# Performance work log

Hardware: AMD Instinct MI355X
Metric: run time of the kernel (lower is better)

Reference implementation:

```python
import jax, jax.numpy as jnp
import numpy as np

N_OBJS = 100          # max detections / scatter buffer size
TOP_K = 100           # top_k_n peaks per channel
KP_THRES = 0.3        # score threshold before NMS
NMS_IOU = 0.5
RESIZE_H, RESIZE_W = 1536.0, 1536.0   # resize_shape (== heatmap HxW here)
H, W = 1536, 1536


def _peak_hms(hms):
    # 3x3 stride-1 SAME max pool; keep only local maxima (Base.apply_max_pool)
    hmax = jax.lax.reduce_window(hms, -jnp.inf, jax.lax.max, (1, 3, 3, 1), (1, 1, 1, 1), 'SAME')
    return jnp.where(hms == hmax, hms, 0.0)


def _top_k_loc(hms, k):
    # per-channel top-k peak coordinates -> [b, c, k, 2] (y, x) int32
    b, h, w, c = hms.shape
    flat = jnp.transpose(hms, (0, 3, 1, 2)).reshape(b, c, h * w)
    _, idx = jax.lax.top_k(flat, k)
    return jnp.stack([idx // w, idx % w], axis=-1).astype(jnp.int32)


def _iou_matrix(boxes):
    # boxes [N,4] = (y1,x1,y2,x2)
    y1, x1, y2, x2 = boxes[:, 0], boxes[:, 1], boxes[:, 2], boxes[:, 3]
    area = jnp.maximum(y2 - y1, 0.0) * jnp.maximum(x2 - x1, 0.0)
    iy1 = jnp.maximum(y1[:, None], y1[None, :]); ix1 = jnp.maximum(x1[:, None], x1[None, :])
    iy2 = jnp.minimum(y2[:, None], y2[None, :]); ix2 = jnp.minimum(x2[:, None], x2[None, :])
    inter = jnp.maximum(iy2 - iy1, 0.0) * jnp.maximum(ix2 - ix1, 0.0)
    union = area[:, None] + area[None, :] - inter
    return inter / jnp.maximum(union, 1e-8)


def _nms_single(boxes, scores):
    # greedy single-class NMS, fixed-size (combined_non_max_suppression equivalent,
    # clip_boxes=False, score_threshold=-inf); padded slots are zeros like TF.
    order = jnp.argsort(-scores)
    boxes, scores = boxes[order], scores[order]
    n = boxes.shape[0]
    iou = _iou_matrix(boxes)
    idxs = jnp.arange(n)

    def step(suppressed, inp):
        i, iou_row = inp
        keep_i = ~suppressed[i]
        return suppressed | (keep_i & (iou_row > NMS_IOU) & (idxs > i)), keep_i

    _, keep = jax.lax.scan(step, jnp.zeros(n, bool), (idxs, iou))
    perm = jnp.argsort(jnp.where(keep, 0, 1))  # stable: compact kept to front, score order preserved
    keep_s = keep[perm]
    out_boxes = jnp.where(keep_s[:, None], boxes[perm], 0.0)
    out_scores = jnp.where(keep_s, scores[perm], 0.0)
    return out_boxes, out_scores, jnp.zeros(n, jnp.float32)


def _forward(obj_heat_map, offset_map, size_maps, origin_shapes):
    resize_shape = jnp.array([RESIZE_H, RESIZE_W], jnp.float32)
    ratio = origin_shapes / resize_shape                      # [b,2]
    hms = _peak_hms(obj_heat_map)                             # [b,H,W,2]
    b = hms.shape[0]
    coors = _top_k_loc(hms, TOP_K)                            # [b,2,K,2]
    b_coors, b_lnmks = coors[:, :1], coors[:, 1:]             # obj / nose coords
    bidx = jnp.arange(b)[:, None, None]

    # nose landmark: scores at nose-channel peaks, masked mean of coords (int mean like TF)
    nose_scores = hms[bidx, b_lnmks[..., 0], b_lnmks[..., 1], 1]     # [b,1,K]
    nose_mask = nose_scores > 0.5
    cnt = jnp.maximum(jnp.sum(nose_mask), 1)
    lnmk_mean = jnp.sum(jnp.where(nose_mask[..., None], b_lnmks, 0), axis=(0, 1, 2)) // cnt
    b_lnmks_m = lnmk_mean.reshape(b, 1, 2)                    # requires b == 1 (as in original)
    b_nose_scores = jnp.where(nose_mask, nose_scores, -1.0).reshape(b, -1)

    # boxes from sizes at object peaks
    size_vals = size_maps[bidx, b_coors[..., 0], b_coors[..., 1]]    # [b,1,K,2]
    obj_scores = hms[bidx, b_coors[..., 0], b_coors[..., 1], 0]      # [b,1,K]
    centers = b_coors.astype(jnp.float32)
    tls = jnp.maximum(centers - size_vals / 2.0, 0.0)
    brs = jnp.minimum(centers + size_vals / 2.0, resize_shape - 1.0)
    bboxes = jnp.concatenate([tls, brs], axis=-1) * jnp.tile(ratio, (1, 2))[:, None, None, :]
    bboxes, scores = bboxes[:, 0], obj_scores[:, 0]           # [b,K,4], [b,K]

    # scatter masked candidates into -1-initialized buffer (tensor_scatter_nd_update equivalent)
    mask = scores > KP_THRES
    cand = jnp.where(mask[..., None], jnp.concatenate([bboxes, scores[..., None]], -1), -1.0)
    cand = jnp.pad(cand, ((0, 0), (0, N_OBJS - TOP_K), (0, 0)), constant_values=-1.0)  # [b,N_OBJS,5]

    nb, ns, nc = jax.vmap(_nms_single)(cand[..., :4], cand[..., 4])
    box_results = jnp.where(nb == -1.0, jnp.inf, nb)
    box_results = jnp.where(box_results == 0.0, jnp.inf, box_results)  # (x - 1 == -1)
    b_bboxes = jnp.concatenate([box_results, ns[..., None], nc[..., None]], axis=-1)  # [b,N_OBJS,6]

    # offset vectors at the mean nose landmark (gather 8ch -> [b,n,4,2])
    bidx2 = jnp.arange(b)[:, None]
    off = offset_map[bidx2, b_lnmks_m[..., 0], b_lnmks_m[..., 1]].reshape(b, 1, 4, 2)
    lf = b_lnmks_m.astype(jnp.float32)
    b_ENM = (lf[:, :, None, :] - off) * ratio[:, None, None, :]
    b_lnmks_out = lf * ratio[:, None, :]
    return b_bboxes, b_lnmks_out, b_ENM, b_nose_scores


def setup_inputs() -> dict:
    key = jax.random.key(0)
    k1, k2, k3 = jax.random.split(key, 3)
    obj_heat_map = jax.random.uniform(k1, (1, H, W, 2), jnp.float32)
    offset_map = jax.random.normal(k2, (1, H, W, 8), jnp.float32) * 8.0
    size_maps = jax.random.uniform(k3, (1, H, W, 2), jnp.float32) * 128.0
    origin_shapes = jnp.array([[1080.0, 1920.0]], jnp.float32)
    return {"obj_heat_map": obj_heat_map, "offset_map": offset_map,
            "size_maps": size_maps, "origin_shapes": origin_shapes}


def reference(obj_heat_map, offset_map, size_maps, origin_shapes):
    return _forward(obj_heat_map, offset_map, size_maps, origin_shapes)
```

## Files before the change

kernel.cpp:

```cpp
#include <hip/hip_runtime.h>
#include <cstdint>

#define IW 1536
#define IH 1536
#define TOPK 100
#define CAPP 327680
#define CAPB 128
#define CAPT 8192
#define BF_INF16 0x7F7Fu

typedef unsigned u32; typedef unsigned long long u64; typedef unsigned short u16;

#define OH1   0
#define OH2   512
#define OSEL  1024
#define OCNT  1032
#define OLB   1040
#define OLT   1552
#define OPK   17936

__device__ __forceinline__ u32 enc16(u32 b){ b &= 0xFFFFu; return (b & 0x8000u) ? ((~b)&0xFFFFu) : (b|0x8000u); }
__device__ __forceinline__ u32 dec16(u32 e){ return (e & 0x8000u) ? (e^0x8000u) : ((~e)&0xFFFFu); }
__device__ __forceinline__ float up16(u32 b){ return __uint_as_float((b&0xFFFFu)<<16); }
__device__ __forceinline__ u16 f2bf(float f){ u32 u=__float_as_uint(f); return (u16)((u + 0x7FFFu + ((u>>16)&1u))>>16); }

__global__ __launch_bounds__(1024) void scan_kernel(const u32* __restrict__ hm, u32* __restrict__ ws){
  __shared__ u32 lh[512];
  __shared__ u32 lbuf[2][1600];
  __shared__ u32 lcnt[2], lbase[2];
  int tid = threadIdx.x, lane = tid & 63;
  for(int i=tid;i<512;i+=1024) lh[i]=0u;
  if(tid<2) lcnt[tid]=0u;
  __syncthreads();

  int p = (blockIdx.x*1024 + tid)*4;
  int y = p / IW, x = p - y*IW;
  const u32* R1 = hm + y*IW;
  const u32* R0 = y ? R1 - IW : R1;
  const u32* R2 = (y < IH-1) ? R1 + IW : R1;
  uint4 c0 = *(const uint4*)(R0+x), c1 = *(const uint4*)(R1+x), c2 = *(const uint4*)(R2+x);
  int xl = x ? x-1 : 0, xr = (x+4 < IW) ? x+4 : IW-1;
  u32 a0[6] = {R0[xl], c0.x, c0.y, c0.z, c0.w, R0[xr]};
  u32 a1[6] = {R1[xl], c1.x, c1.y, c1.z, c1.w, R1[xr]};
  u32 a2[6] = {R2[xl], c2.x, c2.y, c2.z, c2.w, R2[xr]};

  #pragma unroll
  for(int j=0;j<4;++j){
    u32 c = a1[j+1];
    u32 cl = c & 0xFFFFu, chv = c >> 16;
    u32 m0=0u, m1=0u;
    #pragma unroll
    for(int d=0;d<3;++d){
      u32 n0=a0[j+d], n2=a2[j+d];
      u32 t;
      t=n0&0xFFFFu; m0=t>m0?t:m0;  t=n0>>16; m1=t>m1?t:m1;
      t=n2&0xFFFFu; m0=t>m0?t:m0;  t=n2>>16; m1=t>m1?t:m1;
    }
    { u32 n=a1[j]; u32 t=n&0xFFFFu; m0=t>m0?t:m0; t=n>>16; m1=t>m1?t:m1; }
    { u32 n=a1[j+2]; u32 t=n&0xFFFFu; m0=t>m0?t:m0; t=n>>16; m1=t>m1?t:m1; }
    bool p0 = (cl >= m0), p1 = (chv >= m1);

    u64 mk0 = __ballot(p0);
    if(mk0){
      u32 cntw = __popcll(mk0), b;
      if(lane==0) b = atomicAdd(&lcnt[0], cntw);
      b = __shfl(b, 0);
      if(p0){
        u32 pos = b + __popcll(mk0 & ((1ull<<lane)-1ull));
        if(pos < 1600) lbuf[0][pos] = (u32)(p+j);
      }
    }
    u64 mk1 = __ballot(p1);
    if(mk1){
      u32 cntw = __popcll(mk1), b;
      if(lane==0) b = atomicAdd(&lcnt[1], cntw);
      b = __shfl(b, 0);
      if(p1){
        u32 pos = b + __popcll(mk1 & ((1ull<<lane)-1ull));
        if(pos < 1600) lbuf[1][pos] = (u32)(p+j);
      }
    }
    if(p0) atomicAdd(&lh[enc16(cl)>>8], 1u);
    if(p1) atomicAdd(&lh[256 + (enc16(chv)>>8)], 1u);
  }
  __syncthreads();
  if(tid < 2){
    u32 n = lcnt[tid]; if(n > 1600) n = 1600;
    lcnt[tid] = n;
    lbase[tid] = atomicAdd(&ws[OCNT+tid], n);
  }
  __syncthreads();
  for(int ch=0;ch<2;++ch){
    u32 n = lcnt[ch], base = lbase[ch];
    for(u32 i=tid;i<n;i+=1024){
      u32 g = base + i;
      if(g < CAPP) ws[OPK + ch*CAPP + g] = lbuf[ch][i];
    }
  }
  for(int i=tid;i<512;i+=1024) if(lh[i]) atomicAdd(&ws[OH1+i], lh[i]);
}

__global__ void sel_msd_kernel(u32* __restrict__ ws){
  __shared__ u32 h[512];
  int t = threadIdx.x;
  h[t] = ws[OH1+t];
  __syncthreads();
  if(t < 2){
    const u32* hh = h + t*256;
    u32 above = 0; int D = 0;
    for(int b=255;b>=1;--b){
      if(above + hh[b] >= (u32)TOPK){ D = b; break; }
      above += hh[b];
    }
    ws[OSEL+t] = (u32)D;
    ws[OSEL+2+t] = above;
  }
}

__global__ __launch_bounds__(1024) void lsd_kernel(const u32* __restrict__ hm, u32* __restrict__ ws){
  __shared__ u32 lh[512];
  int tid = threadIdx.x;
  for(int i=tid;i<512;i+=1024) lh[i]=0u;
  __syncthreads();
  int D0 = (int)ws[OSEL], D1 = (int)ws[OSEL+1];
  for(int ch=0;ch<2;++ch){
    u32 n = ws[OCNT+ch]; if(n > CAPP) n = CAPP;
    int D = ch ? D1 : D0;
    for(u32 i = blockIdx.x*1024 + tid; i < n; i += gridDim.x*1024){
      u32 idx = ws[OPK + ch*CAPP + i];
      u32 e = enc16(hm[idx] >> (16*ch));
      if((int)(e>>8) == D) atomicAdd(&lh[ch*256 + (e&255)], 1u);
    }
  }
  __syncthreads();
  for(int i=tid;i<512;i+=1024) if(lh[i]) atomicAdd(&ws[OH2+i], lh[i]);
}

__global__ void sel_lsd_kernel(u32* __restrict__ ws){
  __shared__ u32 h[512];
  int t = threadIdx.x;
  h[t] = ws[OH2+t];
  __syncthreads();
  if(t < 2){
    int D = (int)ws[OSEL+t];
    int need2 = TOPK - (int)ws[OSEL+2+t];
    const u32* hh = h + t*256;
    u32 above = 0; int L = 0;
    for(int b=255;b>=1;--b){
      if((int)(above + hh[b]) >= need2){ L = b; break; }
      above += hh[b];
    }
    ws[OSEL+4+t] = (u32)((D<<8) | L);
  }
}

__global__ __launch_bounds__(1024) void collect_kernel(const u32* __restrict__ hm, u32* __restrict__ ws){
  __shared__ u32 tbuf[2][2048];
  __shared__ u32 tcnt[2], tbase[2];
  int tid = threadIdx.x, lane = tid & 63;
  if(tid<2) tcnt[tid]=0u;
  __syncthreads();
  u32 thr0 = ws[OSEL+4], thr1 = ws[OSEL+5];
  u64* listB = (u64*)(ws + OLB);
  u32 total = gridDim.x*1024;
  for(int ch=0;ch<2;++ch){
    u32 n = ws[OCNT+ch]; if(n > CAPP) n = CAPP;
    u32 thr = ch ? thr1 : thr0;
    for(u32 base = blockIdx.x*1024; base < n; base += total){
      u32 i = base + tid;
      bool act = (i < n);
      u32 idx = 0, e = 0;
      if(act){ idx = ws[OPK + ch*CAPP + i]; e = enc16(hm[idx] >> (16*ch)); }
      if(act && e > thr){
        u32 pos = atomicAdd(&ws[OCNT+2+ch], 1u);
        if(pos < CAPB) listB[ch*CAPB + pos] = ((u64)e<<32) | (u32)(~idx);
      }
      bool isT = act && (e == thr);
      u64 mk = __ballot(isT);
      if(mk){
        u32 cntw = __popcll(mk), b;
        if(lane==0) b = atomicAdd(&tcnt[ch], cntw);
        b = __shfl(b, 0);
        if(isT){
          u32 pos = b + __popcll(mk & ((1ull<<lane)-1ull));
          if(pos < 2048) tbuf[ch][pos] = idx;
        }
      }
    }
  }
  __syncthreads();
  if(tid < 2){
    u32 c = tcnt[tid]; if(c > 2048) c = 2048;
    tcnt[tid] = c;
    tbase[tid] = atomicAdd(&ws[OCNT+4+tid], c);
  }
  __syncthreads();
  for(int ch=0;ch<2;++ch)
    for(u32 i=tid;i<tcnt[ch];i+=1024){
      u32 g = tbase[ch] + i;
      if(g < CAPT) ws[OLT + ch*CAPT + g] = tbuf[ch][i];
    }
}

__global__ __launch_bounds__(1024) void finalize_kernel(
    u32* __restrict__ ws, const u32* __restrict__ szm, const u16* __restrict__ offm,
    const u16* __restrict__ orig, u16* __restrict__ out){
  __shared__ u32 cnts[8];
  __shared__ u64 keysL[CAPB];
  __shared__ u32 h2[2048];
  __shared__ u32 wbits[64];
  __shared__ u32 sel[CAPB];
  __shared__ int Bv, cntBelowS, selc;
  __shared__ float oval[TOPK]; __shared__ int oidx[TOPK];
  __shared__ float nval[TOPK]; __shared__ int nidx[TOPK];
  __shared__ float cbox[TOPK][4]; __shared__ float cscore[TOPK]; __shared__ float area[TOPK];
  __shared__ int sup[TOPK]; __shared__ int slotv[TOPK];
  __shared__ u64 nbits[2*TOPK];
  __shared__ u64 suppS[2];
  __shared__ int cS, srS, scS, meanr, meanc;
  int tid = threadIdx.x, lane = tid & 63;
  const u64* listB = (const u64*)(ws + OLB);

  if(tid < 6) cnts[tid] = ws[OCNT+tid];
  if(tid < 2) cnts[6+tid] = ws[OSEL+4+tid];
  if(tid < TOPK){ oval[tid]=0.0f; oidx[tid]=0; nval[tid]=0.0f; nidx[tid]=0; }
  __syncthreads();

  for(int ch=0; ch<2; ++ch){
    int nB = (int)cnts[2+ch]; if(nB > CAPB) nB = CAPB; if(nB > TOPK) nB = TOPK;
    u32 thr = cnts[6+ch];
    float tval = up16(dec16(thr));
    float* dval = ch ? nval : oval;
    int*   didx = ch ? nidx : oidx;

    u64 kreg = 0;
    if(tid < nB){ kreg = listB[ch*CAPB + tid]; keysL[tid] = kreg; }
    for(int i=tid;i<2048;i+=1024) h2[i]=0u;
    if(tid < 64) wbits[tid]=0u;
    if(tid == 0){ selc = 0; Bv = 0; cntBelowS = 0; }
    __syncthreads();
    if(tid < nB){
      int r = 0;
      for(int j=0;j<nB;++j) r += (keysL[j] > kreg);
      dval[r] = up16(dec16((u32)(kreg>>32)));
      didx[r] = (int)(~(u32)(kreg & 0xFFFFFFFFu));
    }
    int need = TOPK - nB;

    if(need > 0){
      int nT = (int)cnts[4+ch]; if(nT > CAPT) nT = CAPT;
      const u32* seg = ws + OLT + ch*CAPT;
      for(int i=tid;i<nT;i+=1024) atomicAdd(&h2[seg[i]>>11], 1u);
      __syncthreads();
      if(tid < 64){
        int base = tid*32;
        u32 s = 0;
        #pragma unroll
        for(int k2=0;k2<32;++k2) s += h2[base+k2];
        u32 c = s;
        #pragma unroll
        for(int off=1;off<64;off<<=1){
          u32 v = __shfl_up(c, off, 64);
          if(lane >= off) c += v;
        }
        u64 m = __ballot(c >= (u32)need);
        int L = (int)(__ffsll((unsigned long long)m) - 1);
        if(tid == L){
          u32 cum2 = c - s;
          int B = base;
          for(int k2=0;k2<32;++k2){
            u32 hb = h2[base+k2];
            if(cum2 + hb >= (u32)need){ B = base+k2; break; }
            cum2 += hb;
          }
          Bv = B; cntBelowS = (int)cum2;
        }
      }
      __syncthreads();
      int B = Bv;
      for(int i=tid;i<nT;i+=1024){
        u32 idx = seg[i];
        int b = (int)(idx>>11);
        if(b < B){
          int pos = atomicAdd(&selc, 1);
          if(pos < CAPB) sel[pos] = idx;
        } else if(b == B){
          atomicOr(&wbits[(idx&2047)>>5], 1u<<(idx&31));
        }
      }
      __syncthreads();
      int sc = selc; if(sc > CAPB) sc = CAPB;
      if(tid < sc){
        u32 v = sel[tid];
        int r = 0;
        for(int j=0;j<sc;++j) r += (sel[j] < v);
        if(nB + r < TOPK){ dval[nB+r] = tval; didx[nB+r] = (int)v; }
      }
      if(tid == 0){
        int rem = need - sc;
        int pos = nB + sc;
        for(int wi=0; wi<64 && rem>0; ++wi){
          u32 bits = wbits[wi];
          while(bits && rem>0){
            int l = __ffs(bits) - 1;
            bits &= bits - 1;
            if(pos < TOPK){ dval[pos] = tval; didx[pos] = (int)(((u32)B<<11) | ((u32)wi<<5) | (u32)l); }
            ++pos; --rem;
          }
        }
      }
    }
    __syncthreads();
  }

  float ry = up16(orig[0]) / 1536.0f;
  float rx = up16(orig[1]) / 1536.0f;

  if(tid == 0){ cS = 0; srS = 0; scS = 0; }
  __syncthreads();
  if(tid < TOPK && nval[tid] > 0.5f){
    atomicAdd(&cS, 1);
    atomicAdd(&srS, nidx[tid] / IW);
    atomicAdd(&scS, nidx[tid] % IW);
  }
  if(tid < TOPK) out[610 + tid] = f2bf(nval[tid] > 0.5f ? nval[tid] : -1.0f);
  __syncthreads();
  if(tid == 0){
    int c = cS < 1 ? 1 : cS;
    meanr = srS / c; meanc = scS / c;
  }

  if(tid < TOPK){
    int idx = oidx[tid];
    int r = idx / IW, c = idx - r*IW;
    float score = oval[tid];
    u32 sz = szm[idx];
    float sy = up16(sz), sx = up16(sz>>16);
    float cy = (float)r, cx = (float)c;
    float tly = fmaxf(cy - sy*0.5f, 0.0f);
    float tlx = fmaxf(cx - sx*0.5f, 0.0f);
    float bry = fminf(cy + sy*0.5f, 1535.0f);
    float brx = fminf(cx + sx*0.5f, 1535.0f);
    bool mk = score > 0.3f;
    float b0 = mk ? tly*ry : -1.0f;
    float b1 = mk ? tlx*rx : -1.0f;
    float b2 = mk ? bry*ry : -1.0f;
    float b3 = mk ? brx*rx : -1.0f;
    cbox[tid][0]=b0; cbox[tid][1]=b1; cbox[tid][2]=b2; cbox[tid][3]=b3;
    cscore[tid] = mk ? score : -1.0f;
    area[tid] = fmaxf(b2-b0,0.0f) * fmaxf(b3-b1,0.0f);
  }
  if(tid < 2*TOPK) nbits[tid] = 0ull;
  __syncthreads();

  for(int t=tid; t<TOPK*TOPK; t+=1024){
    int i = t / TOPK, j = t - i*TOPK;
    if(j > i){
      float iy1 = fmaxf(cbox[i][0], cbox[j][0]);
      float ix1 = fmaxf(cbox[i][1], cbox[j][1]);
      float iy2 = fminf(cbox[i][2], cbox[j][2]);
      float ix2 = fminf(cbox[i][3], cbox[j][3]);
      float inter = fmaxf(iy2-iy1,0.0f) * fmaxf(ix2-ix1,0.0f);
      float uni = (area[i] + area[j]) - inter;
      if(inter / fmaxf(uni, 1e-8f) > 0.5f)
        atomicOr(&nbits[i*2 + (j>>6)], 1ull << (j&63));
    }
  }
  __syncthreads();
  if(tid == 0){
    u64 s0 = 0ull, s1 = 0ull;
    for(int i=0;i<TOPK;++i){
      bool su = (i<64) ? ((s0>>i)&1ull) : ((s1>>(i-64))&1ull);
      if(!su){ s0 |= nbits[i*2]; s1 |= nbits[i*2+1]; }
    }
    suppS[0] = s0; suppS[1] = s1;
  }
  __syncthreads();
  if(tid < TOPK) sup[tid] = (int)((suppS[tid>>6] >> (tid&63)) & 1ull);
  __syncthreads();

  if(tid < TOPK){
    int kbefore = 0, sbefore = 0, ktot = 0;
    for(int j=0;j<TOPK;++j){
      int sj = sup[j];
      ktot += (1 - sj);
      if(j < tid){ kbefore += (1 - sj); sbefore += sj; }
    }
    int slot = sup[tid] ? (ktot + sbefore) : kbefore;
    slotv[slot] = tid;
  }
  __syncthreads();

  if(tid < TOPK){
    int s = slotv[tid];
    bool ks = !sup[s];
    u16 row[6];
    if(ks){
      for(int d=0;d<4;++d){
        float v = cbox[s][d];
        row[d] = (v == -1.0f || v == 0.0f) ? (u16)BF_INF16 : f2bf(v);
      }
      row[4] = f2bf(cscore[s]);
    } else {
      for(int d=0;d<4;++d) row[d] = (u16)BF_INF16;
      row[4] = 0;
    }
    row[5] = 0;
    for(int d=0;d<6;++d) out[tid*6 + d] = row[d];
  }

  if(tid == 0){
    float lfy = (float)meanr, lfx = (float)meanc;
    out[600] = f2bf(lfy * ry);
    out[601] = f2bf(lfx * rx);
    const u16* op = offm + ((size_t)meanr*IW + meanc)*8;
    for(int p=0;p<4;++p){
      out[602 + p*2 + 0] = f2bf((lfy - up16(op[p*2+0])) * ry);
      out[602 + p*2 + 1] = f2bf((lfx - up16(op[p*2+1])) * rx);
    }
  }
}

extern "C" void kernel_launch(void* const* d_in, const int* in_sizes, int n_in,
                              void* d_out, int out_size, void* d_ws, size_t ws_size,
                              hipStream_t stream) {
  const u32* heat = (const u32*)d_in[0];
  const u16* offm = (const u16*)d_in[1];
  const u32* szm  = (const u32*)d_in[2];
  const u16* orig = (const u16*)d_in[3];
  u16* out = (u16*)d_out;
  u32* ws = (u32*)d_ws;

  hipMemsetAsync(ws, 0, 1040*sizeof(u32), stream);
  scan_kernel<<<576, 1024, 0, stream>>>(heat, ws);
  sel_msd_kernel<<<1, 512, 0, stream>>>(ws);
  lsd_kernel<<<128, 1024, 0, stream>>>(heat, ws);
  sel_lsd_kernel<<<1, 512, 0, stream>>>(ws);
  collect_kernel<<<128, 1024, 0, stream>>>(heat, ws);
  finalize_kernel<<<1, 1024, 0, stream>>>(ws, szm, offm, orig, out);
}
```

Before: 195.9 us.

## Fuse six top-k/NMS kernels into one persistent kernel with grid barriers

Replaces the six back-to-back launches (scan, two selection steps, refine histogram, collect, finalize) with a single persistent kernel of 128 blocks that synchronise through an atomic grid barrier in workspace memory. The scan phase loops over chunks and also stores each peak's 16-bit value next to its index, so later phases read a compact value array instead of re-gathering from the heatmap. This removes launch gaps and random heatmap reads, but relies on all 128 blocks being co-resident, and it cuts scan parallelism from 576 blocks to 128.

```diff
diff --git a/kernel.cpp b/kernel.cpp
--- a/kernel.cpp
+++ b/kernel.cpp
@@ -3,6 +3,8 @@
 
 #define IW 1536
 #define IH 1536
+#define NCHUNK 576
+#define GRID 128
 #define TOPK 100
 #define CAPP 327680
 #define CAPB 128
@@ -15,248 +17,266 @@
 #define OH2   512
 #define OSEL  1024
 #define OCNT  1032
+#define OBARA 1038
+#define OBARG 1039
 #define OLB   1040
 #define OLT   1552
 #define OPK   17936
+#define OPV   (OPK + 2*CAPP)
 
 __device__ __forceinline__ u32 enc16(u32 b){ b &= 0xFFFFu; return (b & 0x8000u) ? ((~b)&0xFFFFu) : (b|0x8000u); }
 __device__ __forceinline__ u32 dec16(u32 e){ return (e & 0x8000u) ? (e^0x8000u) : ((~e)&0xFFFFu); }
 __device__ __forceinline__ float up16(u32 b){ return __uint_as_float((b&0xFFFFu)<<16); }
 __device__ __forceinline__ u16 f2bf(float f){ u32 u=__float_as_uint(f); return (u16)((u + 0x7FFFu + ((u>>16)&1u))>>16); }
 
-__global__ __launch_bounds__(1024) void scan_kernel(const u32* __restrict__ hm, u32* __restrict__ ws){
-  __shared__ u32 lh[512];
-  __shared__ u32 lbuf[2][1600];
-  __shared__ u32 lcnt[2], lbase[2];
+__device__ __forceinline__ void gbar(u32* ws, u32 t){
+  __syncthreads();
+  if(threadIdx.x == 0){
+    __threadfence();
+    u32 old = __hip_atomic_fetch_add(ws + OBARA, 1u, __ATOMIC_ACQ_REL, __HIP_MEMORY_SCOPE_AGENT);
+    if(old == (u32)GRID * t - 1u){
+      __hip_atomic_store(ws + OBARG, t, __ATOMIC_RELEASE, __HIP_MEMORY_SCOPE_AGENT);
+    } else {
+      while(__hip_atomic_load(ws + OBARG, __ATOMIC_ACQUIRE, __HIP_MEMORY_SCOPE_AGENT) < t)
+        __builtin_amdgcn_s_sleep(2);
+    }
+  }
+  __syncthreads();
+}
+
+union SMem {
+  struct { u32 lh[512]; u32 lbuf[2][1600]; u16 vbuf[2][1600]; u32 lcnt[2], lbase[2]; } p0;
+  struct { u32 lh[512]; } p2;
+  struct { u32 tbuf[2][2048]; u32 tcnt[2], tbase[2]; } p4;
+  struct {
+    u32 cnts[8];
+    u64 keysL[CAPB];
+    u32 h2[2048];
+    u32 wbits[64];
+    u32 sel[CAPB];
+    int Bv, selc;
+    float oval[TOPK]; int oidx[TOPK];
+    float nval[TOPK]; int nidx[TOPK];
+    float cbox[TOPK][4]; float cscore[TOPK]; float area[TOPK];
+    int sup[TOPK]; int slotv[TOPK];
+    u64 nbits[2*TOPK];
+    u64 suppS[2];
+    int cS, srS, scS, meanr, meanc;
+  } p5;
+};
+
+__global__ __launch_bounds__(1024, 4) void fused_kernel(
+    const u32* __restrict__ hm, u32* __restrict__ ws, const u32* __restrict__ szm,
+    const u16* __restrict__ offm, const u16* __restrict__ orig, u16* __restrict__ out){
+  __shared__ SMem sm;
   int tid = threadIdx.x, lane = tid & 63;
-  for(int i=tid;i<512;i+=1024) lh[i]=0u;
-  if(tid<2) lcnt[tid]=0u;
-  __syncthreads();
-
-  int p = (blockIdx.x*1024 + tid)*4;
-  int y = p / IW, x = p - y*IW;
-  const u32* R1 = hm + y*IW;
-  const u32* R0 = y ? R1 - IW : R1;
-  const u32* R2 = (y < IH-1) ? R1 + IW : R1;
-  uint4 c0 = *(const uint4*)(R0+x), c1 = *(const uint4*)(R1+x), c2 = *(const uint4*)(R2+x);
-  int xl = x ? x-1 : 0, xr = (x+4 < IW) ? x+4 : IW-1;
-  u32 a0[6] = {R0[xl], c0.x, c0.y, c0.z, c0.w, R0[xr]};
-  u32 a1[6] = {R1[xl], c1.x, c1.y, c1.z, c1.w, R1[xr]};
-  u32 a2[6] = {R2[xl], c2.x, c2.y, c2.z, c2.w, R2[xr]};
-
-  #pragma unroll
-  for(int j=0;j<4;++j){
-    u32 c = a1[j+1];
-    u32 cl = c & 0xFFFFu, chv = c >> 16;
-    u32 m0=0u, m1=0u;
+  u16* pv = (u16*)(ws + OPV);
+
+  for(int i=tid;i<512;i+=1024) sm.p0.lh[i]=0u;
+  for(int c = blockIdx.x; c < NCHUNK; c += GRID){
+    if(tid<2) sm.p0.lcnt[tid]=0u;
+    __syncthreads();
+    int p = c*4096 + tid*4;
+    int y = p / IW, x = p - y*IW;
+    const u32* R1 = hm + y*IW;
+    const u32* R0 = y ? R1 - IW : R1;
+    const u32* R2 = (y < IH-1) ? R1 + IW : R1;
+    uint4 c0 = *(const uint4*)(R0+x), c1 = *(const uint4*)(R1+x), c2 = *(const uint4*)(R2+x);
+    int xl = x ? x-1 : 0, xr = (x+4 < IW) ? x+4 : IW-1;
+    u32 a0[6] = {R0[xl], c0.x, c0.y, c0.z, c0.w, R0[xr]};
+    u32 a1[6] = {R1[xl], c1.x, c1.y, c1.z, c1.w, R1[xr]};
+    u32 a2[6] = {R2[xl], c2.x, c2.y, c2.z, c2.w, R2[xr]};
     #pragma unroll
-    for(int d=0;d<3;++d){
-      u32 n0=a0[j+d], n2=a2[j+d];
-      u32 t;
-      t=n0&0xFFFFu; m0=t>m0?t:m0;  t=n0>>16; m1=t>m1?t:m1;
-      t=n2&0xFFFFu; m0=t>m0?t:m0;  t=n2>>16; m1=t>m1?t:m1;
-    }
-    { u32 n=a1[j]; u32 t=n&0xFFFFu; m0=t>m0?t:m0; t=n>>16; m1=t>m1?t:m1; }
-    { u32 n=a1[j+2]; u32 t=n&0xFFFFu; m0=t>m0?t:m0; t=n>>16; m1=t>m1?t:m1; }
-    bool p0 = (cl >= m0), p1 = (chv >= m1);
-
-    u64 mk0 = __ballot(p0);
-    if(mk0){
-      u32 cntw = __popcll(mk0), b;
-      if(lane==0) b = atomicAdd(&lcnt[0], cntw);
-      b = __shfl(b, 0);
-      if(p0){
-        u32 pos = b + __popcll(mk0 & ((1ull<<lane)-1ull));
-        if(pos < 1600) lbuf[0][pos] = (u32)(p+j);
-      }
-    }
-    u64 mk1 = __ballot(p1);
-    if(mk1){
-      u32 cntw = __popcll(mk1), b;
-      if(lane==0) b = atomicAdd(&lcnt[1], cntw);
-      b = __shfl(b, 0);
-      if(p1){
-        u32 pos = b + __popcll(mk1 & ((1ull<<lane)-1ull));
-        if(pos < 1600) lbuf[1][pos] = (u32)(p+j);
-      }
-    }
-    if(p0) atomicAdd(&lh[enc16(cl)>>8], 1u);
-    if(p1) atomicAdd(&lh[256 + (enc16(chv)>>8)], 1u);
-  }
-  __syncthreads();
-  if(tid < 2){
-    u32 n = lcnt[tid]; if(n > 1600) n = 1600;
-    lcnt[tid] = n;
-    lbase[tid] = atomicAdd(&ws[OCNT+tid], n);
-  }
-  __syncthreads();
-  for(int ch=0;ch<2;++ch){
-    u32 n = lcnt[ch], base = lbase[ch];
-    for(u32 i=tid;i<n;i+=1024){
-      u32 g = base + i;
-      if(g < CAPP) ws[OPK + ch*CAPP + g] = lbuf[ch][i];
-    }
-  }
-  for(int i=tid;i<512;i+=1024) if(lh[i]) atomicAdd(&ws[OH1+i], lh[i]);
-}
-
-__global__ void sel_msd_kernel(u32* __restrict__ ws){
-  __shared__ u32 h[512];
-  int t = threadIdx.x;
-  h[t] = ws[OH1+t];
-  __syncthreads();
-  if(t < 2){
-    const u32* hh = h + t*256;
-    u32 above = 0; int D = 0;
-    for(int b=255;b>=1;--b){
-      if(above + hh[b] >= (u32)TOPK){ D = b; break; }
-      above += hh[b];
-    }
-    ws[OSEL+t] = (u32)D;
-    ws[OSEL+2+t] = above;
-  }
-}
-
-__global__ __launch_bounds__(1024) void lsd_kernel(const u32* __restrict__ hm, u32* __restrict__ ws){
-  __shared__ u32 lh[512];
-  int tid = threadIdx.x;
-  for(int i=tid;i<512;i+=1024) lh[i]=0u;
-  __syncthreads();
-  int D0 = (int)ws[OSEL], D1 = (int)ws[OSEL+1];
-  for(int ch=0;ch<2;++ch){
-    u32 n = ws[OCNT+ch]; if(n > CAPP) n = CAPP;
-    int D = ch ? D1 : D0;
-    for(u32 i = blockIdx.x*1024 + tid; i < n; i += gridDim.x*1024){
-      u32 idx = ws[OPK + ch*CAPP + i];
-      u32 e = enc16(hm[idx] >> (16*ch));
-      if((int)(e>>8) == D) atomicAdd(&lh[ch*256 + (e&255)], 1u);
-    }
-  }
-  __syncthreads();
-  for(int i=tid;i<512;i+=1024) if(lh[i]) atomicAdd(&ws[OH2+i], lh[i]);
-}
-
-__global__ void sel_lsd_kernel(u32* __restrict__ ws){
-  __shared__ u32 h[512];
-  int t = threadIdx.x;
-  h[t] = ws[OH2+t];
-  __syncthreads();
-  if(t < 2){
-    int D = (int)ws[OSEL+t];
-    int need2 = TOPK - (int)ws[OSEL+2+t];
-    const u32* hh = h + t*256;
-    u32 above = 0; int L = 0;
-    for(int b=255;b>=1;--b){
-      if((int)(above + hh[b]) >= need2){ L = b; break; }
-      above += hh[b];
-    }
-    ws[OSEL+4+t] = (u32)((D<<8) | L);
-  }
-}
-
-__global__ __launch_bounds__(1024) void collect_kernel(const u32* __restrict__ hm, u32* __restrict__ ws){
-  __shared__ u32 tbuf[2][2048];
-  __shared__ u32 tcnt[2], tbase[2];
-  int tid = threadIdx.x, lane = tid & 63;
-  if(tid<2) tcnt[tid]=0u;
-  __syncthreads();
-  u32 thr0 = ws[OSEL+4], thr1 = ws[OSEL+5];
-  u64* listB = (u64*)(ws + OLB);
-  u32 total = gridDim.x*1024;
-  for(int ch=0;ch<2;++ch){
-    u32 n = ws[OCNT+ch]; if(n > CAPP) n = CAPP;
-    u32 thr = ch ? thr1 : thr0;
-    for(u32 base = blockIdx.x*1024; base < n; base += total){
-      u32 i = base + tid;
-      bool act = (i < n);
-      u32 idx = 0, e = 0;
-      if(act){ idx = ws[OPK + ch*CAPP + i]; e = enc16(hm[idx] >> (16*ch)); }
-      if(act && e > thr){
-        u32 pos = atomicAdd(&ws[OCNT+2+ch], 1u);
-        if(pos < CAPB) listB[ch*CAPB + pos] = ((u64)e<<32) | (u32)(~idx);
-      }
-      bool isT = act && (e == thr);
-      u64 mk = __ballot(isT);
-      if(mk){
-        u32 cntw = __popcll(mk), b;
-        if(lane==0) b = atomicAdd(&tcnt[ch], cntw);
+    for(int j=0;j<4;++j){
+      u32 cc = a1[j+1];
+      u32 cl = cc & 0xFFFFu, chv = cc >> 16;
+      u32 m0=0u, m1=0u;
+      #pragma unroll
+      for(int d=0;d<3;++d){
+        u32 n0=a0[j+d], n2=a2[j+d]; u32 t;
+        t=n0&0xFFFFu; m0=t>m0?t:m0;  t=n0>>16; m1=t>m1?t:m1;
+        t=n2&0xFFFFu; m0=t>m0?t:m0;  t=n2>>16; m1=t>m1?t:m1;
+      }
+      { u32 n=a1[j];   u32 t=n&0xFFFFu; m0=t>m0?t:m0; t=n>>16; m1=t>m1?t:m1; }
+      { u32 n=a1[j+2]; u32 t=n&0xFFFFu; m0=t>m0?t:m0; t=n>>16; m1=t>m1?t:m1; }
+      bool pk0 = (cl >= m0), pk1 = (chv >= m1);
+      u32 idx = (u32)(p + j);
+      u64 mk0 = __ballot(pk0);
+      if(mk0){
+        u32 cw = __popcll(mk0), b;
+        if(lane==0) b = atomicAdd(&sm.p0.lcnt[0], cw);
         b = __shfl(b, 0);
-        if(isT){
-          u32 pos = b + __popcll(mk & ((1ull<<lane)-1ull));
-          if(pos < 2048) tbuf[ch][pos] = idx;
-        }
-      }
-    }
-  }
-  __syncthreads();
-  if(tid < 2){
-    u32 c = tcnt[tid]; if(c > 2048) c = 2048;
-    tcnt[tid] = c;
-    tbase[tid] = atomicAdd(&ws[OCNT+4+tid], c);
-  }
-  __syncthreads();
-  for(int ch=0;ch<2;++ch)
-    for(u32 i=tid;i<tcnt[ch];i+=1024){
-      u32 g = tbase[ch] + i;
-      if(g < CAPT) ws[OLT + ch*CAPT + g] = tbuf[ch][i];
-    }
-}
-
-__global__ __launch_bounds__(1024) void finalize_kernel(
-    u32* __restrict__ ws, const u32* __restrict__ szm, const u16* __restrict__ offm,
-    const u16* __restrict__ orig, u16* __restrict__ out){
-  __shared__ u32 cnts[8];
-  __shared__ u64 keysL[CAPB];
-  __shared__ u32 h2[2048];
-  __shared__ u32 wbits[64];
-  __shared__ u32 sel[CAPB];
-  __shared__ int Bv, cntBelowS, selc;
-  __shared__ float oval[TOPK]; __shared__ int oidx[TOPK];
-  __shared__ float nval[TOPK]; __shared__ int nidx[TOPK];
-  __shared__ float cbox[TOPK][4]; __shared__ float cscore[TOPK]; __shared__ float area[TOPK];
-  __shared__ int sup[TOPK]; __shared__ int slotv[TOPK];
-  __shared__ u64 nbits[2*TOPK];
-  __shared__ u64 suppS[2];
-  __shared__ int cS, srS, scS, meanr, meanc;
-  int tid = threadIdx.x, lane = tid & 63;
+        if(pk0){
+          u32 pos = b + __popcll(mk0 & ((1ull<<lane)-1ull));
+          if(pos < 1600){ sm.p0.lbuf[0][pos] = idx; sm.p0.vbuf[0][pos] = (u16)cl; }
+        }
+      }
+      u64 mk1 = __ballot(pk1);
+      if(mk1){
+        u32 cw = __popcll(mk1), b;
+        if(lane==0) b = atomicAdd(&sm.p0.lcnt[1], cw);
+        b = __shfl(b, 0);
+        if(pk1){
+          u32 pos = b + __popcll(mk1 & ((1ull<<lane)-1ull));
+          if(pos < 1600){ sm.p0.lbuf[1][pos] = idx; sm.p0.vbuf[1][pos] = (u16)chv; }
+        }
+      }
+      if(pk0) atomicAdd(&sm.p0.lh[enc16(cl)>>8], 1u);
+      if(pk1) atomicAdd(&sm.p0.lh[256 + (enc16(chv)>>8)], 1u);
+    }
+    __syncthreads();
+    if(tid < 2){
+      u32 n = sm.p0.lcnt[tid]; if(n > 1600) n = 1600;
+      sm.p0.lcnt[tid] = n;
+      sm.p0.lbase[tid] = atomicAdd(&ws[OCNT+tid], n);
+    }
+    __syncthreads();
+    for(int ch=0;ch<2;++ch){
+      u32 n = sm.p0.lcnt[ch], base = sm.p0.lbase[ch];
+      for(u32 i=tid;i<n;i+=1024){
+        u32 g = base + i;
+        if(g < CAPP){ ws[OPK + ch*CAPP + g] = sm.p0.lbuf[ch][i]; pv[ch*CAPP + g] = sm.p0.vbuf[ch][i]; }
+      }
+    }
+    __syncthreads();
+  }
+  for(int i=tid;i<512;i+=1024) if(sm.p0.lh[i]) atomicAdd(&ws[OH1+i], sm.p0.lh[i]);
+  gbar(ws, 1);
+
+  if(blockIdx.x == 0){
+    if(tid < 512) sm.p2.lh[tid] = ws[OH1+tid];
+    __syncthreads();
+    if(tid < 2){
+      const u32* hh = sm.p2.lh + tid*256;
+      u32 above = 0; int D = 0;
+      for(int b=255;b>=1;--b){
+        if(above + hh[b] >= (u32)TOPK){ D = b; break; }
+        above += hh[b];
+      }
+      ws[OSEL+tid] = (u32)D;
+      ws[OSEL+2+tid] = above;
+    }
+  }
+  gbar(ws, 2);
+
+  {
+    for(int i=tid;i<512;i+=1024) sm.p2.lh[i]=0u;
+    __syncthreads();
+    int D0 = (int)ws[OSEL], D1 = (int)ws[OSEL+1];
+    for(int ch=0;ch<2;++ch){
+      u32 n = ws[OCNT+ch]; if(n > CAPP) n = CAPP;
+      int D = ch ? D1 : D0;
+      for(u32 i = blockIdx.x*1024 + tid; i < n; i += GRID*1024){
+        u32 e = enc16(pv[ch*CAPP + i]);
+        if((int)(e>>8) == D) atomicAdd(&sm.p2.lh[ch*256 + (e&255)], 1u);
+      }
+    }
+    __syncthreads();
+    for(int i=tid;i<512;i+=1024) if(sm.p2.lh[i]) atomicAdd(&ws[OH2+i], sm.p2.lh[i]);
+  }
+  gbar(ws, 3);
+
+  if(blockIdx.x == 0){
+    if(tid < 512) sm.p2.lh[tid] = ws[OH2+tid];
+    __syncthreads();
+    if(tid < 2){
+      int D = (int)ws[OSEL+tid];
+      int need2 = TOPK - (int)ws[OSEL+2+tid];
+      const u32* hh = sm.p2.lh + tid*256;
+      u32 above = 0; int L = 0;
+      for(int b=255;b>=1;--b){
+        if((int)(above + hh[b]) >= need2){ L = b; break; }
+        above += hh[b];
+      }
+      ws[OSEL+4+tid] = (u32)((D<<8) | L);
+    }
+  }
+  gbar(ws, 4);
+
+  {
+    if(tid<2) sm.p4.tcnt[tid]=0u;
+    __syncthreads();
+    u32 thr0 = ws[OSEL+4], thr1 = ws[OSEL+5];
+    u64* listB = (u64*)(ws + OLB);
+    for(int ch=0;ch<2;++ch){
+      u32 n = ws[OCNT+ch]; if(n > CAPP) n = CAPP;
+      u32 thr = ch ? thr1 : thr0;
+      for(u32 base = blockIdx.x*1024; base < n; base += GRID*1024){
+        u32 i = base + tid;
+        bool act = (i < n);
+        u32 idx = 0, e = 0;
+        if(act){ idx = ws[OPK + ch*CAPP + i]; e = enc16(pv[ch*CAPP + i]); }
+        if(act && e > thr){
+          u32 pos = atomicAdd(&ws[OCNT+2+ch], 1u);
+          if(pos < CAPB) listB[ch*CAPB + pos] = ((u64)e<<32) | (u32)(~idx);
+        }
+        bool isT = act && (e == thr);
+        u64 mk = __ballot(isT);
+        if(mk){
+          u32 cw = __popcll(mk), b;
+          if(lane==0) b = atomicAdd(&sm.p4.tcnt[ch], cw);
+          b = __shfl(b, 0);
+          if(isT){
+            u32 pos = b + __popcll(mk & ((1ull<<lane)-1ull));
+            if(pos < 2048) sm.p4.tbuf[ch][pos] = idx;
+          }
+        }
+      }
+    }
+    __syncthreads();
+    if(tid < 2){
+      u32 c = sm.p4.tcnt[tid]; if(c > 2048) c = 2048;
+      sm.p4.tcnt[tid] = c;
+      sm.p4.tbase[tid] = atomicAdd(&ws[OCNT+4+tid], c);
+    }
+    __syncthreads();
+    for(int ch=0;ch<2;++ch)
+      for(u32 i=tid;i<sm.p4.tcnt[ch];i+=1024){
+        u32 g = sm.p4.tbase[ch] + i;
+        if(g < CAPT) ws[OLT + ch*CAPT + g] = sm.p4.tbuf[ch][i];
+      }
+  }
+  gbar(ws, 5);
+
+  if(blockIdx.x != 0) return;
   const u64* listB = (const u64*)(ws + OLB);
 
-  if(tid < 6) cnts[tid] = ws[OCNT+tid];
-  if(tid < 2) cnts[6+tid] = ws[OSEL+4+tid];
-  if(tid < TOPK){ oval[tid]=0.0f; oidx[tid]=0; nval[tid]=0.0f; nidx[tid]=0; }
+  if(tid < 6) sm.p5.cnts[tid] = ws[OCNT+tid];
+  if(tid < 2) sm.p5.cnts[6+tid] = ws[OSEL+4+tid];
+  if(tid < TOPK){ sm.p5.oval[tid]=0.0f; sm.p5.oidx[tid]=0; sm.p5.nval[tid]=0.0f; sm.p5.nidx[tid]=0; }
   __syncthreads();
 
   for(int ch=0; ch<2; ++ch){
-    int nB = (int)cnts[2+ch]; if(nB > CAPB) nB = CAPB; if(nB > TOPK) nB = TOPK;
-    u32 thr = cnts[6+ch];
+    int nB = (int)sm.p5.cnts[2+ch]; if(nB > CAPB) nB = CAPB; if(nB > TOPK) nB = TOPK;
+    u32 thr = sm.p5.cnts[6+ch];
     float tval = up16(dec16(thr));
-    float* dval = ch ? nval : oval;
-    int*   didx = ch ? nidx : oidx;
+    float* dval = ch ? sm.p5.nval : sm.p5.oval;
+    int*   didx = ch ? sm.p5.nidx : sm.p5.oidx;
 
     u64 kreg = 0;
-    if(tid < nB){ kreg = listB[ch*CAPB + tid]; keysL[tid] = kreg; }
-    for(int i=tid;i<2048;i+=1024) h2[i]=0u;
-    if(tid < 64) wbits[tid]=0u;
-    if(tid == 0){ selc = 0; Bv = 0; cntBelowS = 0; }
+    if(tid < nB){ kreg = listB[ch*CAPB + tid]; sm.p5.keysL[tid] = kreg; }
+    for(int i=tid;i<2048;i+=1024) sm.p5.h2[i]=0u;
+    if(tid < 64) sm.p5.wbits[tid]=0u;
+    if(tid == 0){ sm.p5.selc = 0; sm.p5.Bv = 0; }
     __syncthreads();
     if(tid < nB){
       int r = 0;
-      for(int j=0;j<nB;++j) r += (keysL[j] > kreg);
+      for(int j=0;j<nB;++j) r += (sm.p5.keysL[j] > kreg);
       dval[r] = up16(dec16((u32)(kreg>>32)));
       didx[r] = (int)(~(u32)(kreg & 0xFFFFFFFFu));
     }
     int need = TOPK - nB;
 
     if(need > 0){
-      int nT = (int)cnts[4+ch]; if(nT > CAPT) nT = CAPT;
+      int nT = (int)sm.p5.cnts[4+ch]; if(nT > CAPT) nT = CAPT;
       const u32* seg = ws + OLT + ch*CAPT;
-      for(int i=tid;i<nT;i+=1024) atomicAdd(&h2[seg[i]>>11], 1u);
+      for(int i=tid;i<nT;i+=1024) atomicAdd(&sm.p5.h2[seg[i]>>11], 1u);
       __syncthreads();
       if(tid < 64){
         int base = tid*32;
         u32 s = 0;
         #pragma unroll
-        for(int k2=0;k2<32;++k2) s += h2[base+k2];
+        for(int k2=0;k2<32;++k2) s += sm.p5.h2[base+k2];
         u32 c = s;
         #pragma unroll
         for(int off=1;off<64;off<<=1){
@@ -269,38 +289,38 @@
           u32 cum2 = c - s;
           int B = base;
           for(int k2=0;k2<32;++k2){
-            u32 hb = h2[base+k2];
+            u32 hb = sm.p5.h2[base+k2];
             if(cum2 + hb >= (u32)need){ B = base+k2; break; }
             cum2 += hb;
           }
-          Bv = B; cntBelowS = (int)cum2;
+          sm.p5.Bv = B;
         }
       }
       __syncthreads();
-      int B = Bv;
+      int B = sm.p5.Bv;
       for(int i=tid;i<nT;i+=1024){
         u32 idx = seg[i];
         int b = (int)(idx>>11);
         if(b < B){
-          int pos = atomicAdd(&selc, 1);
-          if(pos < CAPB) sel[pos] = idx;
+          int pos = atomicAdd(&sm.p5.selc, 1);
+          if(pos < CAPB) sm.p5.sel[pos] = idx;
         } else if(b == B){
-          atomicOr(&wbits[(idx&2047)>>5], 1u<<(idx&31));
+          atomicOr(&sm.p5.wbits[(idx&2047)>>5], 1u<<(idx&31));
         }
       }
       __syncthreads();
-      int sc = selc; if(sc > CAPB) sc = CAPB;
+      int sc = sm.p5.selc; if(sc > CAPB) sc = CAPB;
       if(tid < sc){
-        u32 v = sel[tid];
+        u32 v = sm.p5.sel[tid];
         int r = 0;
-        for(int j=0;j<sc;++j) r += (sel[j] < v);
+        for(int j=0;j<sc;++j) r += (sm.p5.sel[j] < v);
         if(nB + r < TOPK){ dval[nB+r] = tval; didx[nB+r] = (int)v; }
       }
       if(tid == 0){
         int rem = need - sc;
         int pos = nB + sc;
         for(int wi=0; wi<64 && rem>0; ++wi){
-          u32 bits = wbits[wi];
+          u32 bits = sm.p5.wbits[wi];
           while(bits && rem>0){
             int l = __ffs(bits) - 1;
             bits &= bits - 1;
@@ -316,24 +336,24 @@
   float ry = up16(orig[0]) / 1536.0f;
   float rx = up16(orig[1]) / 1536.0f;
 
-  if(tid == 0){ cS = 0; srS = 0; scS = 0; }
-  __syncthreads();
-  if(tid < TOPK && nval[tid] > 0.5f){
-    atomicAdd(&cS, 1);
-    atomicAdd(&srS, nidx[tid] / IW);
-    atomicAdd(&scS, nidx[tid] % IW);
-  }
-  if(tid < TOPK) out[610 + tid] = f2bf(nval[tid] > 0.5f ? nval[tid] : -1.0f);
+  if(tid == 0){ sm.p5.cS = 0; sm.p5.srS = 0; sm.p5.scS = 0; }
+  __syncthreads();
+  if(tid < TOPK && sm.p5.nval[tid] > 0.5f){
+    atomicAdd(&sm.p5.cS, 1);
+    atomicAdd(&sm.p5.srS, sm.p5.nidx[tid] / IW);
+    atomicAdd(&sm.p5.scS, sm.p5.nidx[tid] % IW);
+  }
+  if(tid < TOPK) out[610 + tid] = f2bf(sm.p5.nval[tid] > 0.5f ? sm.p5.nval[tid] : -1.0f);
   __syncthreads();
   if(tid == 0){
-    int c = cS < 1 ? 1 : cS;
-    meanr = srS / c; meanc = scS / c;
+    int c = sm.p5.cS < 1 ? 1 : sm.p5.cS;
+    sm.p5.meanr = sm.p5.srS / c; sm.p5.meanc = sm.p5.scS / c;
   }
 
   if(tid < TOPK){
-    int idx = oidx[tid];
+    int idx = sm.p5.oidx[tid];
     int r = idx / IW, c = idx - r*IW;
-    float score = oval[tid];
+    float score = sm.p5.oval[tid];
     u32 sz = szm[idx];
     float sy = up16(sz), sx = up16(sz>>16);
     float cy = (float)r, cx = (float)c;
@@ -346,24 +366,24 @@
     float b1 = mk ? tlx*rx : -1.0f;
     float b2 = mk ? bry*ry : -1.0f;
     float b3 = mk ? brx*rx : -1.0f;
-    cbox[tid][0]=b0; cbox[tid][1]=b1; cbox[tid][2]=b2; cbox[tid][3]=b3;
-    cscore[tid] = mk ? score : -1.0f;
-    area[tid] = fmaxf(b2-b0,0.0f) * fmaxf(b3-b1,0.0f);
-  }
-  if(tid < 2*TOPK) nbits[tid] = 0ull;
+    sm.p5.cbox[tid][0]=b0; sm.p5.cbox[tid][1]=b1; sm.p5.cbox[tid][2]=b2; sm.p5.cbox[tid][3]=b3;
+    sm.p5.cscore[tid] = mk ? score : -1.0f;
+    sm.p5.area[tid] = fmaxf(b2-b0,0.0f) * fmaxf(b3-b1,0.0f);
+  }
+  if(tid < 2*TOPK) sm.p5.nbits[tid] = 0ull;
   __syncthreads();
 
   for(int t=tid; t<TOPK*TOPK; t+=1024){
     int i = t / TOPK, j = t - i*TOPK;
     if(j > i){
-      float iy1 = fmaxf(cbox[i][0], cbox[j][0]);
-      float ix1 = fmaxf(cbox[i][1], cbox[j][1]);
-      float iy2 = fminf(cbox[i][2], cbox[j][2]);
-      float ix2 = fminf(cbox[i][3], cbox[j][3]);
+      float iy1 = fmaxf(sm.p5.cbox[i][0], sm.p5.cbox[j][0]);
+      float ix1 = fmaxf(sm.p5.cbox[i][1], sm.p5.cbox[j][1]);
+      float iy2 = fminf(sm.p5.cbox[i][2], sm.p5.cbox[j][2]);
+      float ix2 = fminf(sm.p5.cbox[i][3], sm.p5.cbox[j][3]);
       float inter = fmaxf(iy2-iy1,0.0f) * fmaxf(ix2-ix1,0.0f);
-      float uni = (area[i] + area[j]) - inter;
+      float uni = (sm.p5.area[i] + sm.p5.area[j]) - inter;
       if(inter / fmaxf(uni, 1e-8f) > 0.5f)
-        atomicOr(&nbits[i*2 + (j>>6)], 1ull << (j&63));
+        atomicOr(&sm.p5.nbits[i*2 + (j>>6)], 1ull << (j&63));
     }
   }
   __syncthreads();
@@ -371,36 +391,36 @@
     u64 s0 = 0ull, s1 = 0ull;
     for(int i=0;i<TOPK;++i){
       bool su = (i<64) ? ((s0>>i)&1ull) : ((s1>>(i-64))&1ull);
-      if(!su){ s0 |= nbits[i*2]; s1 |= nbits[i*2+1]; }
-    }
-    suppS[0] = s0; suppS[1] = s1;
-  }
-  __syncthreads();
-  if(tid < TOPK) sup[tid] = (int)((suppS[tid>>6] >> (tid&63)) & 1ull);
+      if(!su){ s0 |= sm.p5.nbits[i*2]; s1 |= sm.p5.nbits[i*2+1]; }
+    }
+    sm.p5.suppS[0] = s0; sm.p5.suppS[1] = s1;
+  }
+  __syncthreads();
+  if(tid < TOPK) sm.p5.sup[tid] = (int)((sm.p5.suppS[tid>>6] >> (tid&63)) & 1ull);
   __syncthreads();
 
   if(tid < TOPK){
     int kbefore = 0, sbefore = 0, ktot = 0;
     for(int j=0;j<TOPK;++j){
-      int sj = sup[j];
+      int sj = sm.p5.sup[j];
       ktot += (1 - sj);
       if(j < tid){ kbefore += (1 - sj); sbefore += sj; }
     }
-    int slot = sup[tid] ? (ktot + sbefore) : kbefore;
-    slotv[slot] = tid;
+    int slot = sm.p5.sup[tid] ? (ktot + sbefore) : kbefore;
+    sm.p5.slotv[slot] = tid;
   }
   __syncthreads();
 
   if(tid < TOPK){
-    int s = slotv[tid];
-    bool ks = !sup[s];
+    int s = sm.p5.slotv[tid];
+    bool ks = !sm.p5.sup[s];
     u16 row[6];
     if(ks){
       for(int d=0;d<4;++d){
-        float v = cbox[s][d];
+        float v = sm.p5.cbox[s][d];
         row[d] = (v == -1.0f || v == 0.0f) ? (u16)BF_INF16 : f2bf(v);
       }
-      row[4] = f2bf(cscore[s]);
+      row[4] = f2bf(sm.p5.cscore[s]);
     } else {
       for(int d=0;d<4;++d) row[d] = (u16)BF_INF16;
       row[4] = 0;
@@ -410,10 +430,10 @@
   }
 
   if(tid == 0){
-    float lfy = (float)meanr, lfx = (float)meanc;
+    float lfy = (float)sm.p5.meanr, lfx = (float)sm.p5.meanc;
     out[600] = f2bf(lfy * ry);
     out[601] = f2bf(lfx * rx);
-    const u16* op = offm + ((size_t)meanr*IW + meanc)*8;
+    const u16* op = offm + ((size_t)sm.p5.meanr*IW + sm.p5.meanc)*8;
     for(int p=0;p<4;++p){
       out[602 + p*2 + 0] = f2bf((lfy - up16(op[p*2+0])) * ry);
       out[602 + p*2 + 1] = f2bf((lfx - up16(op[p*2+1])) * rx);
@@ -432,10 +452,5 @@
   u32* ws = (u32*)d_ws;
 
   hipMemsetAsync(ws, 0, 1040*sizeof(u32), stream);
-  scan_kernel<<<576, 1024, 0, stream>>>(heat, ws);
-  sel_msd_kernel<<<1, 512, 0, stream>>>(ws);
-  lsd_kernel<<<128, 1024, 0, stream>>>(heat, ws);
-  sel_lsd_kernel<<<1, 512, 0, stream>>>(ws);
-  collect_kernel<<<128, 1024, 0, stream>>>(heat, ws);
-  finalize_kernel<<<1, 1024, 0, stream>>>(ws, szm, offm, orig, out);
+  fused_kernel<<<GRID, 1024, 0, stream>>>(heat, ws, szm, offm, orig, out);
 }
```

Result: slower. 246.9 us (+26.1%).
